# Kernel tuning notes

Hardware: AMD Instinct MI355X
Metric: run time of the kernel (lower is better)

## Reference

```python
import jax, jax.numpy as jnp
import numpy as np

N = 50000          # nodes
E = 800000         # edges per graph view
D_IN = 256
D_HID = 128
N_CLS = 40
EPS = 1e-12


def agnn_conv(x, src, dst, beta):
    """DGL AGNNConv: cosine edge attention + edge softmax + weighted aggregation."""
    # L2-normalize node features (F.normalize, eps=1e-12)
    norm = jnp.sqrt(jnp.sum(x * x, axis=1, keepdims=True))
    hn = x / jnp.maximum(norm, EPS)                      # [N, D]
    # cosine similarity per edge, scaled by learned beta
    e = beta * jnp.sum(hn[src] * hn[dst], axis=1)        # [E]
    # segment (per-destination) stable softmax
    m = jax.ops.segment_max(e, dst, num_segments=N)      # [N]
    m = jnp.where(jnp.isfinite(m), m, 0.0)               # empty segments -> -inf
    ee = jnp.exp(e - m[dst])                             # [E]
    s = jax.ops.segment_sum(ee, dst, num_segments=N)     # [N]
    a = ee / jnp.maximum(s[dst], EPS)                    # [E]
    # weighted sparse aggregation of ORIGINAL (un-normalized) features
    return jax.ops.segment_sum(a[:, None] * x[src], dst, num_segments=N)


def setup_inputs() -> dict:
    key = jax.random.key(0)
    ks = jax.random.split(key, 10)
    return {
        "input_features": jax.random.normal(ks[0], (N, D_IN), dtype=jnp.float32),
        "src1": jax.random.randint(ks[1], (E,), 0, N, dtype=jnp.int32),
        "dst1": jax.random.randint(ks[2], (E,), 0, N, dtype=jnp.int32),
        "src2": jax.random.randint(ks[3], (E,), 0, N, dtype=jnp.int32),
        "dst2": jax.random.randint(ks[4], (E,), 0, N, dtype=jnp.int32),
        "order_attn": jax.random.uniform(ks[5], (2,), dtype=jnp.float32),
        "W1": jax.random.normal(ks[6], (D_IN, D_HID), dtype=jnp.float32) * (2.0 / np.sqrt(D_IN + D_HID)),
        "b1": jnp.zeros((D_HID,), dtype=jnp.float32),
        "W2": jax.random.normal(ks[7], (D_HID, N_CLS), dtype=jnp.float32) * (2.0 / np.sqrt(D_HID + N_CLS)),
        "b2": jnp.zeros((N_CLS,), dtype=jnp.float32),
        "beta1": jnp.ones((), dtype=jnp.float32),
        "beta2": jnp.ones((), dtype=jnp.float32),
    }


def reference(input_features, src1, dst1, src2, dst2, order_attn, W1, b1, W2, b2, beta1, beta2):
    # fc1 + relu
    x1 = jax.nn.relu(input_features @ W1 + b1)           # [N, D_HID]
    # layer1 over both graph views, combined by learned order_attn scalars
    x2 = order_attn[0] * agnn_conv(x1, src1, dst1, beta1) \
       + order_attn[1] * agnn_conv(x1, src2, dst2, beta1)
    # layer2 over both views
    x3 = order_attn[0] * agnn_conv(x2, src1, dst1, beta2) \
       + order_attn[1] * agnn_conv(x2, src2, dst2, beta2)
    # fc2 (original computes F.log_softmax but discards it; returns logits)
    return x3 @ W2 + b2                                   # [N, N_CLS]
```

## Files before the change

### kernel.cpp

```cpp
#include <hip/hip_runtime.h>
#include <hip/hip_fp16.h>
#include <math.h>

#define NNODES 50000
#define NEDGES 800000
#define DIN    256
#define DHID   128
#define NCLS   40

#define BW    128
#define NBK   391
#define CAP   6144
#define PPART 128
#define CHUNK 6250

union HF8 { float4 f; __half2 h2[4]; };

__global__ __launch_bounds__(256) void fc1_kernel(
    const float* __restrict__ X, const float* __restrict__ W1,
    const float* __restrict__ b1, __half* __restrict__ x1h,
    float* __restrict__ inv1)
{
  __shared__ float Xs[16][DIN];
  __shared__ float ssrow[16];
  const int tid   = threadIdx.x;
  const int node0 = blockIdx.x * 16;

  if (tid < 16) ssrow[tid] = 0.f;
  const float4* Xv  = (const float4*)(X + (size_t)node0 * DIN);
  float4*       Xsv = (float4*)(&Xs[0][0]);
#pragma unroll
  for (int t = 0; t < 4; ++t) Xsv[tid + t * 256] = Xv[tid + t * 256];
  __syncthreads();

  const int h  = tid & 127;
  const int tm = tid >> 7;
  float acc[8];
#pragma unroll
  for (int r = 0; r < 8; ++r) acc[r] = 0.f;

  for (int k = 0; k < DIN; k += 4) {
    const float w0 = W1[(k + 0) * DHID + h];
    const float w1 = W1[(k + 1) * DHID + h];
    const float w2 = W1[(k + 2) * DHID + h];
    const float w3 = W1[(k + 3) * DHID + h];
#pragma unroll
    for (int r = 0; r < 8; ++r) {
      const float4 xv = *(const float4*)&Xs[tm * 8 + r][k];
      acc[r] += xv.x * w0 + xv.y * w1 + xv.z * w2 + xv.w * w3;
    }
  }
  const float bb   = b1[h];
  const int   lane = tid & 63;
#pragma unroll
  for (int r = 0; r < 8; ++r) {
    float v = acc[r] + bb;
    v = v > 0.f ? v : 0.f;
    x1h[(size_t)(node0 + tm * 8 + r) * DHID + h] = __float2half(v);
    float q = v * v;
#pragma unroll
    for (int off = 32; off; off >>= 1) q += __shfl_xor(q, off);
    if (lane == 0) atomicAdd(&ssrow[tm * 8 + r], q);
  }
  __syncthreads();
  if (tid < 16) inv1[node0 + tid] = 1.0f / fmaxf(sqrtf(ssrow[tid]), 1e-12f);
}

__global__ __launch_bounds__(320) void fc2_kernel(
    const float* __restrict__ x3, const float* __restrict__ W2,
    const float* __restrict__ b2, float* __restrict__ out)
{
  __shared__ float Xs[8][DHID];
  const int tid   = threadIdx.x;
  const int node0 = blockIdx.x * 8;
  for (int idx = tid; idx < 8 * DHID; idx += 320)
    Xs[idx >> 7][idx & 127] = x3[(size_t)node0 * DHID + idx];
  __syncthreads();

  const int ns = tid / NCLS;
  const int c  = tid - ns * NCLS;
  float acc = b2[c];
#pragma unroll 8
  for (int k = 0; k < DHID; ++k) acc += Xs[ns][k] * W2[k * NCLS + c];
  out[(size_t)(node0 + ns) * NCLS + c] = acc;
}

__global__ __launch_bounds__(256) void hist_part_kernel(
    const int* __restrict__ dst1, const int* __restrict__ dst2,
    int* __restrict__ H)
{
  const int bid = blockIdx.x;
  const int v   = bid >= PPART;
  const int p   = v ? bid - PPART : bid;
  const int* __restrict__ dst = v ? dst2 : dst1;

  __shared__ int hist[NBK];
  for (int i = threadIdx.x; i < NBK; i += 256) hist[i] = 0;
  __syncthreads();
  const int beg = p * CHUNK;
  const int end = (beg + CHUNK < NEDGES) ? beg + CHUNK : NEDGES;
  for (int j = beg + threadIdx.x; j < end; j += 256)
    atomicAdd(&hist[dst[j] >> 7], 1);
  __syncthreads();
  for (int i = threadIdx.x; i < NBK; i += 256)
    H[(v * NBK + i) * PPART + p] = hist[i];
}

__global__ __launch_bounds__(128) void scan_bucket_kernel(
    int* __restrict__ H, int* __restrict__ btot)
{
  const int b   = blockIdx.x;
  const int tid = threadIdx.x;
  __shared__ int sm[PPART];
  const int v = H[b * PPART + tid];
  sm[tid] = v;
  __syncthreads();
  for (int off = 1; off < PPART; off <<= 1) {
    int t = (tid >= off) ? sm[tid - off] : 0;
    __syncthreads();
    sm[tid] += t;
    __syncthreads();
  }
  H[b * PPART + tid] = sm[tid] - v;
  if (tid == PPART - 1) btot[b] = sm[tid];
}

__global__ __launch_bounds__(1024) void scan_btot_kernel(
    const int* __restrict__ btot, int* __restrict__ boffG)
{
  __shared__ int sm[1024];
  const int tid = threadIdx.x;
  const int v = (tid < 2 * NBK) ? btot[tid] : 0;
  sm[tid] = v;
  __syncthreads();
  for (int off = 1; off < 1024; off <<= 1) {
    int t = (tid >= off) ? sm[tid - off] : 0;
    __syncthreads();
    sm[tid] += t;
    __syncthreads();
  }
  if (tid < 2 * NBK) boffG[tid] = sm[tid] - v;
  if (tid == 0) boffG[2 * NBK] = 2 * NEDGES;
}

__global__ __launch_bounds__(256) void scatter_part_kernel(
    const int* __restrict__ src1, const int* __restrict__ dst1,
    const int* __restrict__ src2, const int* __restrict__ dst2,
    const int* __restrict__ H, const int* __restrict__ boffG,
    int2* __restrict__ st)
{
  const int bid = blockIdx.x;
  const int v   = bid >= PPART;
  const int p   = v ? bid - PPART : bid;
  const int* __restrict__ src = v ? src2 : src1;
  const int* __restrict__ dst = v ? dst2 : dst1;

  __shared__ int lcur[NBK];
  for (int i = threadIdx.x; i < NBK; i += 256)
    lcur[i] = boffG[v * NBK + i] + H[(v * NBK + i) * PPART + p];
  __syncthreads();
  const int beg = p * CHUNK;
  const int end = (beg + CHUNK < NEDGES) ? beg + CHUNK : NEDGES;
  for (int j = beg + threadIdx.x; j < end; j += 256) {
    const int s = src[j], d = dst[j];
    const int k = atomicAdd(&lcur[d >> 7], 1);
    st[k] = make_int2(s, d);
  }
}

__global__ __launch_bounds__(256) void build_buckets_kernel(
    const int2* __restrict__ st, const int* __restrict__ boffG,
    int* __restrict__ rp1, int* __restrict__ rp2,
    int* __restrict__ col1, int* __restrict__ col2)
{
  const int bid = blockIdx.x;
  const int v   = bid >= NBK;
  const int b   = v ? bid - NBK : bid;
  int* __restrict__ rp  = v ? rp2 : rp1;
  int* __restrict__ col = v ? col2 : col1;
  const int tid = threadIdx.x;

  const int off0G  = boffG[bid];
  const int cnt    = boffG[bid + 1] - off0G;
  const int off0   = off0G - v * NEDGES;
  const int base_d = b * BW;
  const int nd     = (NNODES - base_d < BW) ? (NNODES - base_d) : BW;

  __shared__ int deg[BW];
  __shared__ int loff[BW + 1];
  __shared__ int cur[BW];
  __shared__ int lcol[CAP];

  if (tid < BW) deg[tid] = 0;
  __syncthreads();
  for (int j = tid; j < cnt; j += 256)
    atomicAdd(&deg[st[off0G + j].y - base_d], 1);
  __syncthreads();

  if (tid == 0) loff[0] = 0;
  if (tid < BW) loff[tid + 1] = deg[tid];
  __syncthreads();
  for (int off = 1; off < BW; off <<= 1) {
    int t = (tid < BW && tid + 1 >= off) ? loff[tid + 1 - off] : 0;
    __syncthreads();
    if (tid < BW && tid + 1 >= off) loff[tid + 1] += t;
    __syncthreads();
  }
  if (tid < nd) rp[base_d + tid] = off0 + loff[tid];
  if (tid == 0 && b == NBK - 1) rp[NNODES] = NEDGES;
  if (tid < BW) cur[tid] = loff[tid];
  __syncthreads();

  if (cnt <= CAP) {
    for (int j = tid; j < cnt; j += 256) {
      const int2 pr = st[off0G + j];
      const int k = atomicAdd(&cur[pr.y - base_d], 1);
      lcol[k] = pr.x;
    }
    __syncthreads();
    if (tid < nd) {
      const int s0 = loff[tid], s1 = s0 + deg[tid];
      for (int a = s0 + 1; a < s1; ++a) {
        const int key = lcol[a];
        int c = a - 1;
        while (c >= s0 && lcol[c] > key) { lcol[c + 1] = lcol[c]; --c; }
        lcol[c + 1] = key;
      }
    }
    __syncthreads();
    for (int j = tid; j < cnt; j += 256) col[off0 + j] = lcol[j];
  } else {
    for (int j = tid; j < cnt; j += 256) {
      const int2 pr = st[off0G + j];
      const int k = atomicAdd(&cur[pr.y - base_d], 1);
      col[off0 + k] = pr.x;
    }
    __syncthreads();
    if (tid < nd) {
      const int s0 = off0 + loff[tid], s1 = s0 + deg[tid];
      for (int a = s0 + 1; a < s1; ++a) {
        const int key = col[a];
        int c = a - 1;
        while (c >= s0 && col[c] > key) { col[c + 1] = col[c]; --c; }
        col[c + 1] = key;
      }
    }
  }
}

__global__ __launch_bounds__(256) void agnn_layer_kernel(
    const __half* __restrict__ xh, const float* __restrict__ inv,
    const int* __restrict__ rp1, const int* __restrict__ col1,
    const int* __restrict__ rp2, const int* __restrict__ col2,
    const float* __restrict__ beta_p, const float* __restrict__ order_attn,
    __half* __restrict__ yh_out, float* __restrict__ inv_out,
    float* __restrict__ y32_out, int n)
{
  const int wid  = (blockIdx.x * blockDim.x + threadIdx.x) >> 6;
  if (wid >= n) return;
  const int lane = threadIdx.x & 63;
  const int grp  = lane >> 4;
  const int sub  = lane & 15;

  const float beta = beta_p[0];
  const float bi   = beta * inv[wid];

  HF8 ud; ud.f = *(const float4*)(xh + (size_t)wid * DHID + sub * 8);
  float xd[8];
#pragma unroll
  for (int i = 0; i < 4; ++i) {
    const float2 t = __half22float2(ud.h2[i]);
    xd[2 * i] = t.x; xd[2 * i + 1] = t.y;
  }

  const int beg1 = rp1[wid], end1 = rp1[wid + 1];
  const int beg2 = rp2[wid], end2 = rp2[wid + 1];

  float s1 = 0.f, s2 = 0.f;
  float y1[8], y2[8];
#pragma unroll
  for (int k = 0; k < 8; ++k) { y1[k] = 0.f; y2[k] = 0.f; }

  int j1 = beg1 + grp, j2 = beg2 + grp;
  int sa1 = col1[j1 < end1 ? j1 : 0];
  int sa2 = col2[j2 < end2 ? j2 : 0];

  while (j1 < end1 || j2 < end2) {
    const bool p1 = j1 < end1;
    const bool p2 = j2 < end2;
    const int  c1 = sa1, c2 = sa2;

    const float isa1 = inv[c1];
    const float isa2 = inv[c2];
    HF8 u1; u1.f = *(const float4*)(xh + (size_t)c1 * DHID + sub * 8);
    HF8 u2; u2.f = *(const float4*)(xh + (size_t)c2 * DHID + sub * 8);

    const int nj1 = j1 + 4, nj2 = j2 + 4;
    sa1 = col1[nj1 < end1 ? nj1 : 0];
    sa2 = col2[nj2 < end2 ? nj2 : 0];

    float av[8], bv[8];
#pragma unroll
    for (int i = 0; i < 4; ++i) {
      const float2 ta = __half22float2(u1.h2[i]);
      const float2 tb = __half22float2(u2.h2[i]);
      av[2 * i] = ta.x; av[2 * i + 1] = ta.y;
      bv[2 * i] = tb.x; bv[2 * i + 1] = tb.y;
    }

    float d1 = 0.f, d2 = 0.f;
#pragma unroll
    for (int k = 0; k < 8; ++k) { d1 += av[k] * xd[k]; d2 += bv[k] * xd[k]; }
#pragma unroll
    for (int off = 1; off <= 8; off <<= 1) {
      d1 += __shfl_xor(d1, off);
      d2 += __shfl_xor(d2, off);
    }

    const float w1 = p1 ? __expf(bi * isa1 * d1) : 0.f;
    const float w2 = p2 ? __expf(bi * isa2 * d2) : 0.f;
    s1 += w1; s2 += w2;
#pragma unroll
    for (int k = 0; k < 8; ++k) {
      y1[k] += w1 * av[k];
      y2[k] += w2 * bv[k];
    }

    j1 = nj1; j2 = nj2;
  }

  s1 += __shfl_xor(s1, 16); s1 += __shfl_xor(s1, 32);
  s2 += __shfl_xor(s2, 16); s2 += __shfl_xor(s2, 32);
#pragma unroll
  for (int k = 0; k < 8; ++k) {
    y1[k] += __shfl_xor(y1[k], 16); y1[k] += __shfl_xor(y1[k], 32);
    y2[k] += __shfl_xor(y2[k], 16); y2[k] += __shfl_xor(y2[k], 32);
  }

  const float r1 = (end1 > beg1) ? order_attn[0] / fmaxf(s1, 1e-12f) : 0.f;
  const float r2 = (end2 > beg2) ? order_attn[1] / fmaxf(s2, 1e-12f) : 0.f;
  float acc[8];
#pragma unroll
  for (int k = 0; k < 8; ++k) acc[k] = r1 * y1[k] + r2 * y2[k];

  if (inv_out) {
    float ss = 0.f;
#pragma unroll
    for (int k = 0; k < 8; ++k) ss += acc[k] * acc[k];
    ss += __shfl_xor(ss, 1);
    ss += __shfl_xor(ss, 2);
    ss += __shfl_xor(ss, 4);
    ss += __shfl_xor(ss, 8);
    if (lane == 0) inv_out[wid] = 1.0f / fmaxf(sqrtf(ss), 1e-12f);
  }

  if (grp == 0) {
    if (yh_out) {
      HF8 o;
      o.h2[0] = __floats2half2_rn(acc[0], acc[1]);
      o.h2[1] = __floats2half2_rn(acc[2], acc[3]);
      o.h2[2] = __floats2half2_rn(acc[4], acc[5]);
      o.h2[3] = __floats2half2_rn(acc[6], acc[7]);
      *(float4*)(yh_out + (size_t)wid * DHID + sub * 8) = o.f;
    }
    if (y32_out) {
      float* yp = y32_out + (size_t)wid * DHID + sub * 8;
      *(float4*)(yp)     = make_float4(acc[0], acc[1], acc[2], acc[3]);
      *(float4*)(yp + 4) = make_float4(acc[4], acc[5], acc[6], acc[7]);
    }
  }
}

extern "C" void kernel_launch(void* const* d_in, const int* in_sizes, int n_in,
                              void* d_out, int out_size, void* d_ws, size_t ws_size,
                              hipStream_t stream)
{
  const float* X          = (const float*)d_in[0];
  const int*   src1       = (const int*)d_in[1];
  const int*   dst1       = (const int*)d_in[2];
  const int*   src2       = (const int*)d_in[3];
  const int*   dst2       = (const int*)d_in[4];
  const float* order_attn = (const float*)d_in[5];
  const float* W1         = (const float*)d_in[6];
  const float* b1         = (const float*)d_in[7];
  const float* W2         = (const float*)d_in[8];
  const float* b2         = (const float*)d_in[9];
  const float* beta1      = (const float*)d_in[10];
  const float* beta2      = (const float*)d_in[11];
  float*       out        = (float*)d_out;

  char*  ws  = (char*)d_ws;
  size_t off = 0;
  auto alloc = [&](size_t bytes) -> void* {
    void* p = ws + off;
    off += (bytes + 255) & ~size_t(255);
    return p;
  };
  __half* x1h  = (__half*)alloc((size_t)NNODES * DHID * 2);
  __half* x2h  = (__half*)alloc((size_t)NNODES * DHID * 2);
  float*  x3   = (float*)alloc((size_t)NNODES * DHID * 4);
  float*  inv1 = (float*)alloc((size_t)NNODES * 4);
  float*  inv2 = (float*)alloc((size_t)NNODES * 4);
  int*    rp1  = (int*)alloc((size_t)(NNODES + 1) * 4);
  int*    rp2  = (int*)alloc((size_t)(NNODES + 1) * 4);
  int*    col1 = (int*)alloc((size_t)NEDGES * 4);
  int*    col2 = (int*)alloc((size_t)NEDGES * 4);
  int*    H    = (int*)alloc((size_t)2 * NBK * PPART * 4);
  int*    btot = (int*)alloc((size_t)2 * NBK * 4);
  int*    boffG= (int*)alloc((size_t)(2 * NBK + 1) * 4);
  int2*   st   = (int2*)x3;

  const int WB = (NNODES + 3) / 4;

  hist_part_kernel<<<2 * PPART, 256, 0, stream>>>(dst1, dst2, H);
  scan_bucket_kernel<<<2 * NBK, 128, 0, stream>>>(H, btot);
  scan_btot_kernel<<<1, 1024, 0, stream>>>(btot, boffG);
  scatter_part_kernel<<<2 * PPART, 256, 0, stream>>>(src1, dst1, src2, dst2,
                                                     H, boffG, st);
  build_buckets_kernel<<<2 * NBK, 256, 0, stream>>>(st, boffG, rp1, rp2, col1, col2);

  fc1_kernel<<<NNODES / 16, 256, 0, stream>>>(X, W1, b1, x1h, inv1);

  agnn_layer_kernel<<<WB, 256, 0, stream>>>(x1h, inv1, rp1, col1, rp2, col2,
                                            beta1, order_attn,
                                            x2h, inv2, nullptr, NNODES);
  agnn_layer_kernel<<<WB, 256, 0, stream>>>(x2h, inv2, rp1, col1, rp2, col2,
                                            beta2, order_attn,
                                            nullptr, nullptr, x3, NNODES);

  fc2_kernel<<<NNODES / 8, 320, 0, stream>>>(x3, W2, b2, out);
}
```

Baseline: 336.6 us.

## Rewrite fc1 as shared-memory tiled GEMM with 4x8 register blocking

Replaces the fc1 kernel, which had each thread compute 8 rows and stream W1 from global memory, with a 64-node by 128-column tiled GEMM. A transposed X tile and a W1 tile are staged in LDS per 64-wide K step, and each thread accumulates a 4x8 output block. Output is written as packed half values and the row norm is reduced across the 16 column threads with shuffles. This cuts global W1 traffic and raises arithmetic intensity, at the cost of more LDS, padding-based transposed stores, and bounds handling for the partial last block.

```diff
diff --git a/kernel.cpp b/kernel.cpp
--- a/kernel.cpp
+++ b/kernel.cpp
@@ -15,55 +15,93 @@
 #define CHUNK 6250
 
 union HF8 { float4 f; __half2 h2[4]; };
+union HF4 { float2 f; __half2 h2[2]; };
 
 __global__ __launch_bounds__(256) void fc1_kernel(
     const float* __restrict__ X, const float* __restrict__ W1,
     const float* __restrict__ b1, __half* __restrict__ x1h,
     float* __restrict__ inv1)
 {
-  __shared__ float Xs[16][DIN];
-  __shared__ float ssrow[16];
+  __shared__ float As[64][65];
+  __shared__ float Bs[64][132];
   const int tid   = threadIdx.x;
-  const int node0 = blockIdx.x * 16;
-
-  if (tid < 16) ssrow[tid] = 0.f;
-  const float4* Xv  = (const float4*)(X + (size_t)node0 * DIN);
-  float4*       Xsv = (float4*)(&Xs[0][0]);
-#pragma unroll
-  for (int t = 0; t < 4; ++t) Xsv[tid + t * 256] = Xv[tid + t * 256];
-  __syncthreads();
-
-  const int h  = tid & 127;
-  const int tm = tid >> 7;
-  float acc[8];
-#pragma unroll
-  for (int r = 0; r < 8; ++r) acc[r] = 0.f;
-
-  for (int k = 0; k < DIN; k += 4) {
-    const float w0 = W1[(k + 0) * DHID + h];
-    const float w1 = W1[(k + 1) * DHID + h];
-    const float w2 = W1[(k + 2) * DHID + h];
-    const float w3 = W1[(k + 3) * DHID + h];
-#pragma unroll
-    for (int r = 0; r < 8; ++r) {
-      const float4 xv = *(const float4*)&Xs[tm * 8 + r][k];
-      acc[r] += xv.x * w0 + xv.y * w1 + xv.z * w2 + xv.w * w3;
-    }
-  }
-  const float bb   = b1[h];
-  const int   lane = tid & 63;
-#pragma unroll
-  for (int r = 0; r < 8; ++r) {
-    float v = acc[r] + bb;
-    v = v > 0.f ? v : 0.f;
-    x1h[(size_t)(node0 + tm * 8 + r) * DHID + h] = __float2half(v);
-    float q = v * v;
-#pragma unroll
-    for (int off = 32; off; off >>= 1) q += __shfl_xor(q, off);
-    if (lane == 0) atomicAdd(&ssrow[tm * 8 + r], q);
-  }
-  __syncthreads();
-  if (tid < 16) inv1[node0 + tid] = 1.0f / fmaxf(sqrtf(ssrow[tid]), 1e-12f);
+  const int node0 = blockIdx.x * 64;
+  const int tx    = tid & 15;
+  const int ty    = tid >> 4;
+
+  const int ml   = tid >> 2;
+  const int kq   = tid & 3;
+  const int mrow = (node0 + ml < NNODES) ? node0 + ml : NNODES - 1;
+
+  float acc[4][8];
+#pragma unroll
+  for (int i = 0; i < 4; ++i)
+#pragma unroll
+    for (int j = 0; j < 8; ++j) acc[i][j] = 0.f;
+
+  for (int kt = 0; kt < 4; ++kt) {
+    const int k0 = kt * 64;
+#pragma unroll
+    for (int q = 0; q < 4; ++q) {
+      const int kk = kq * 16 + q * 4;
+      const float4 v = *(const float4*)(X + (size_t)mrow * DIN + k0 + kk);
+      As[kk + 0][ml] = v.x; As[kk + 1][ml] = v.y;
+      As[kk + 2][ml] = v.z; As[kk + 3][ml] = v.w;
+    }
+#pragma unroll
+    for (int q = 0; q < 8; ++q) {
+      const int flat = q * 1024 + tid * 4;
+      const int kk = flat >> 7, nn = flat & 127;
+      *(float4*)&Bs[kk][nn] = *(const float4*)(W1 + (size_t)(k0 + kk) * DHID + nn);
+    }
+    __syncthreads();
+
+#pragma unroll 4
+    for (int k = 0; k < 64; ++k) {
+      const float4 a  = *(const float4*)&As[k][ty * 4];
+      const float4 b0 = *(const float4*)&Bs[k][tx * 4];
+      const float4 b1v= *(const float4*)&Bs[k][64 + tx * 4];
+      const float av[4] = {a.x, a.y, a.z, a.w};
+      const float bv[8] = {b0.x, b0.y, b0.z, b0.w, b1v.x, b1v.y, b1v.z, b1v.w};
+#pragma unroll
+      for (int i = 0; i < 4; ++i)
+#pragma unroll
+        for (int j = 0; j < 8; ++j) acc[i][j] += av[i] * bv[j];
+    }
+    __syncthreads();
+  }
+
+  const float4 bb0 = *(const float4*)(b1 + tx * 4);
+  const float4 bb1 = *(const float4*)(b1 + 64 + tx * 4);
+  const float bias[8] = {bb0.x, bb0.y, bb0.z, bb0.w, bb1.x, bb1.y, bb1.z, bb1.w};
+
+#pragma unroll
+  for (int i = 0; i < 4; ++i) {
+    const int row = node0 + ty * 4 + i;
+    float v[8];
+    float q = 0.f;
+#pragma unroll
+    for (int j = 0; j < 8; ++j) {
+      float t = acc[i][j] + bias[j];
+      t = t > 0.f ? t : 0.f;
+      v[j] = t;
+      q += t * t;
+    }
+    q += __shfl_xor(q, 1);
+    q += __shfl_xor(q, 2);
+    q += __shfl_xor(q, 4);
+    q += __shfl_xor(q, 8);
+    if (row < NNODES) {
+      HF4 o0, o1;
+      o0.h2[0] = __floats2half2_rn(v[0], v[1]);
+      o0.h2[1] = __floats2half2_rn(v[2], v[3]);
+      o1.h2[0] = __floats2half2_rn(v[4], v[5]);
+      o1.h2[1] = __floats2half2_rn(v[6], v[7]);
+      *(float2*)(x1h + (size_t)row * DHID + tx * 4)      = o0.f;
+      *(float2*)(x1h + (size_t)row * DHID + 64 + tx * 4) = o1.f;
+      if (tx == 0) inv1[row] = 1.0f / fmaxf(sqrtf(q), 1e-12f);
+    }
+  }
 }
 
 __global__ __launch_bounds__(320) void fc2_kernel(
@@ -419,7 +457,7 @@
                                                      H, boffG, st);
   build_buckets_kernel<<<2 * NBK, 256, 0, stream>>>(st, boffG, rp1, rp2, col1, col2);
 
-  fc1_kernel<<<NNODES / 16, 256, 0, stream>>>(X, W1, b1, x1h, inv1);
+  fc1_kernel<<<(NNODES + 63) / 64, 256, 0, stream>>>(X, W1, b1, x1h, inv1);
 
   agnn_layer_kernel<<<WB, 256, 0, stream>>>(x1h, inv1, rp1, col1, rp2, col2,
                                             beta1, order_attn,
```

Result: faster. 304.0 us (-9.7%).
